# Optimization experiments

Measured on AMD Instinct MI355X. Metric: run time of the kernel, lower is better.

Reference implementation:

```python
import jax, jax.numpy as jnp
import numpy as np

NH = 16
NKV = 4
ROPE_BASE = 10000.0
ROPE_TSL = 1024
EPS = 1.1920928955078125e-07  # torch fp32 finfo eps (F.rms_norm default)


def _rms_norm(t):
    return t * jax.lax.rsqrt(jnp.mean(t * t, axis=-1, keepdims=True) + EPS)


def _rope_tables(T, hd):
    # Rotary with rd = hd (rope_dims=0 -> full-head rope). NTK rescale if T > tsl.
    rd = hd
    if T > ROPE_TSL:
        base = ROPE_BASE * (T / ROPE_TSL) ** (rd / (rd - 2))
    else:
        base = ROPE_BASE
    inv_freq = 1.0 / base ** (np.arange(0, rd, 2, dtype=np.float32) / rd)
    t = np.arange(T, dtype=np.float32)
    fr = np.outer(t, inv_freq)  # [T, hd//2]
    return jnp.asarray(np.cos(fr)), jnp.asarray(np.sin(fr))


def _apply_rope(x, cos, sin):
    # x: [B,T,H,D]; cos/sin: [T, D//2] broadcast over batch & heads
    h = x.shape[-1] // 2
    x1, x2 = x[..., :h], x[..., h:]
    c = cos[None, :, None, :]
    s = sin[None, :, None, :]
    return jnp.concatenate((x1 * c + x2 * s, -x1 * s + x2 * c), axis=-1)


def setup_inputs() -> dict:
    key = jax.random.key(0)
    k1, k2, k3, k4, k5 = jax.random.split(key, 5)
    B, T, dim = 2, 2048, 2048
    hd = dim // NH
    kd = NKV * hd
    std = 0.02
    return {
        "x": jax.random.normal(k1, (B, T, dim), dtype=jnp.float32),
        "Wq": jax.random.normal(k2, (dim, dim), dtype=jnp.float32) * std,
        "Wk": jax.random.normal(k3, (kd, dim), dtype=jnp.float32) * std,
        "Wv": jax.random.normal(k4, (kd, dim), dtype=jnp.float32) * std,
        "Wp": jax.random.normal(k5, (dim, dim), dtype=jnp.float32) * std,
        "q_gain": jnp.full((NH,), 1.5, dtype=jnp.float32),
    }


def reference(x, Wq, Wk, Wv, Wp, q_gain):
    B, T, d = x.shape
    hd = d // NH
    g = NH // NKV
    q = (x @ Wq.T).reshape(B, T, NH, hd)
    k = (x @ Wk.T).reshape(B, T, NKV, hd)
    v = (x @ Wv.T).reshape(B, T, NKV, hd)
    q = _rms_norm(q)
    k = _rms_norm(k)
    cos, sin = _rope_tables(T, hd)
    q = _apply_rope(q, cos, sin)
    k = _apply_rope(k, cos, sin)
    q = q * q_gain[None, None, :, None]
    # GQA causal SDPA: group queries per kv head
    qg = q.reshape(B, T, NKV, g, hd)
    scores = jnp.einsum("btkgd,bskd->bkgts", qg, k) / jnp.sqrt(jnp.asarray(hd, x.dtype))
    causal = jnp.tril(jnp.ones((T, T), dtype=bool))
    scores = jnp.where(causal[None, None, None, :, :], scores, jnp.asarray(-jnp.inf, scores.dtype))
    attn = jax.nn.softmax(scores, axis=-1)
    y = jnp.einsum("bkgts,bskd->btkgd", attn, v).reshape(B, T, d)
    return y @ Wp.T
```

## Files before the change

kernel.cpp:

```cpp
#include <hip/hip_runtime.h>
#include <math.h>

#define NH 16
#define NKV 4
#define HD 128
#define DIM 2048
#define GQ 4
#define EPS 1.1920928955078125e-07f

typedef unsigned short u16;
using bf16x8 = __attribute__((ext_vector_type(8))) short;
using f16x4  = __attribute__((ext_vector_type(4))) _Float16;
using f32x4  = __attribute__((ext_vector_type(4))) float;

__device__ inline float fast_exp2(float x) { return __builtin_amdgcn_exp2f(x); }

__device__ inline short f2bf(float f) {
    unsigned u = __builtin_bit_cast(unsigned, f);
    return (short)((u + 0x7FFFu + ((u >> 16) & 1u)) >> 16);
}
__device__ inline u16 f2h(float f) {
    _Float16 h = (_Float16)f;
    return __builtin_bit_cast(u16, h);
}

#define ASYNC_LOAD16(g, l)                                                        \
    __builtin_amdgcn_global_load_lds(                                             \
        (const __attribute__((address_space(1))) unsigned*)(g),                   \
        (__attribute__((address_space(3))) unsigned*)(l), 16, 0, 0)

#define SCHED_FENCE() __builtin_amdgcn_sched_barrier(0)
#define WAIT_LGKM0()  asm volatile("s_waitcnt lgkmcnt(0)" ::: "memory")
#define WAIT_VM(N)    asm volatile("s_waitcnt vmcnt(" #N ")" ::: "memory")

__global__ __launch_bounds__(256) void cvt_fused(
    const float* __restrict__ x,  const float* __restrict__ wq,
    const float* __restrict__ wk, const float* __restrict__ wv,
    const float* __restrict__ wp,
    u16* __restrict__ x16, u16* __restrict__ wqkv, u16* __restrict__ wp16,
    float* __restrict__ ct, float* __restrict__ st, float l2b64,
    int nx4, int total, int nblk_cvt) {
    if ((int)blockIdx.x >= nblk_cvt) {
        const int idx = (blockIdx.x - nblk_cvt) * 256 + threadIdx.x;
        const int t = idx >> 6;
        const int j = idx & 63;
        const float inv_freq = fast_exp2(-(float)j * l2b64);
        const float fr = (float)t * inv_freq;
        ct[idx] = cosf(fr);
        st[idx] = sinf(fr);
        return;
    }
    int i = blockIdx.x * 256 + threadIdx.x;
    if (i >= total) return;
    const int nw4 = DIM * DIM / 4;
    const int nk4 = (NKV * HD) * DIM / 4;
    const float4* s4;
    ushort4* d4;
    if (i < nx4) {
        s4 = (const float4*)x + i; d4 = (ushort4*)x16 + i;
    } else {
        int j = i - nx4;
        if (j < nw4) {
            s4 = (const float4*)wq + j; d4 = (ushort4*)wqkv + j;
        } else {
            j -= nw4;
            if (j < nk4) {
                s4 = (const float4*)wk + j;
                d4 = (ushort4*)wqkv + (size_t)2048 * DIM / 4 + j;
            } else {
                j -= nk4;
                if (j < nk4) {
                    s4 = (const float4*)wv + j;
                    d4 = (ushort4*)wqkv + (size_t)2560 * DIM / 4 + j;
                } else {
                    j -= nk4;
                    s4 = (const float4*)wp + j; d4 = (ushort4*)wp16 + j;
                }
            }
        }
    }
    float4 f = *s4;
    ushort4 o;
    o.x = (u16)f2bf(f.x); o.y = (u16)f2bf(f.y);
    o.z = (u16)f2bf(f.z); o.w = (u16)f2bf(f.w);
    *d4 = o;
}

#define BN 256
#define BKT 64
#define NKT (DIM / BKT)

template <int EPI, int MT>
__global__ __launch_bounds__(512, 2) void gemm256(
    const u16* __restrict__ A, const u16* __restrict__ W,
    float* __restrict__ C, int N,
    u16* __restrict__ q16, u16* __restrict__ k16,
    u16* __restrict__ vt16,
    const float* __restrict__ ctab, const float* __restrict__ stab,
    const float* __restrict__ q_gain, int T) {
    __shared__ u16 As[2][MT * 64 * BKT];
    __shared__ u16 Bs[2][BN * BKT];

    const int tid  = threadIdx.x;
    const int wid  = tid >> 6;
    const int lane = tid & 63;
    const int l16  = lane & 15;
    const int quad = lane >> 4;
    const int wm   = wid >> 1;
    const int wn   = wid & 1;
    const int m0   = blockIdx.x * (MT * 64);
    const int n0   = blockIdx.y * BN;
    const int K    = DIM;

    const int srow = lane >> 3;
    const int scol = ((lane & 7) ^ srow) * 8;
    const u16* pa = A + (size_t)(m0 + srow) * K + scol;
    const u16* pw = W + (size_t)(n0 + srow) * K + scol;

    const int ca0 = ((quad)     ^ (l16 & 7)) * 8;
    const int ca1 = ((4 + quad) ^ (l16 & 7)) * 8;

    f32x4 acc[MT][8];
#pragma unroll
    for (int i = 0; i < MT; i++)
#pragma unroll
        for (int j = 0; j < 8; j++) acc[i][j] = (f32x4){0.f, 0.f, 0.f, 0.f};

#pragma unroll
    for (int r = 0; r < MT; r++)
        ASYNC_LOAD16(pa + (size_t)(r * 64 + wid * 8) * K, &As[0][(r * 64 + wid * 8) * BKT]);
    ASYNC_LOAD16(pw + (size_t)(0 * 64 + wid * 8) * K, &Bs[0][(0 * 64 + wid * 8) * BKT]);
    ASYNC_LOAD16(pw + (size_t)(2 * 64 + wid * 8) * K, &Bs[0][(2 * 64 + wid * 8) * BKT]);
    ASYNC_LOAD16(pw + (size_t)(1 * 64 + wid * 8) * K, &Bs[0][(1 * 64 + wid * 8) * BKT]);
    ASYNC_LOAD16(pw + (size_t)(3 * 64 + wid * 8) * K, &Bs[0][(3 * 64 + wid * 8) * BKT]);
    WAIT_VM(2);
    SCHED_FENCE();
    __builtin_amdgcn_s_barrier();
    SCHED_FENCE();

#pragma unroll 1
    for (int kt = 0; kt < NKT; kt++) {
        const int cur = kt & 1;
        const u16* Ac = &As[cur][0];
        const u16* Bc = &Bs[cur][0];
        u16* An = &As[cur ^ 1][0];
        u16* Bn = &Bs[cur ^ 1][0];
        const size_t ko = (size_t)((kt + 1) & (NKT - 1)) * BKT;

        bf16x8 a0[MT], a1[MT];

        {
            bf16x8 bf[4];
#pragma unroll
            for (int mt = 0; mt < MT; mt++)
                a0[mt] = *(const bf16x8*)&Ac[(wm * (MT * 16) + mt * 16 + l16) * BKT + ca0];
#pragma unroll
            for (int nt = 0; nt < 4; nt++)
                bf[nt] = *(const bf16x8*)&Bc[(wn * 128 + nt * 16 + l16) * BKT + ca0];
#pragma unroll
            for (int r = 0; r < MT; r++)
                ASYNC_LOAD16(pa + (size_t)(r * 64 + wid * 8) * K + ko,
                             &An[(r * 64 + wid * 8) * BKT]);
            SCHED_FENCE();
            __builtin_amdgcn_s_barrier();
            WAIT_LGKM0();
            SCHED_FENCE();
            __builtin_amdgcn_s_setprio(1);
#pragma unroll
            for (int mt = 0; mt < MT; mt++)
#pragma unroll
                for (int nt = 0; nt < 4; nt++)
                    acc[mt][nt] = __builtin_amdgcn_mfma_f32_16x16x32_bf16(
                        a0[mt], bf[nt], acc[mt][nt], 0, 0, 0);
            __builtin_amdgcn_s_setprio(0);
        }

        {
            bf16x8 bf[4];
#pragma unroll
            for (int mt = 0; mt < MT; mt++)
                a1[mt] = *(const bf16x8*)&Ac[(wm * (MT * 16) + mt * 16 + l16) * BKT + ca1];
#pragma unroll
            for (int nt = 0; nt < 4; nt++)
                bf[nt] = *(const bf16x8*)&Bc[(wn * 128 + nt * 16 + l16) * BKT + ca1];
            ASYNC_LOAD16(pw + (size_t)(0 * 64 + wid * 8) * K + ko,
                         &Bn[(0 * 64 + wid * 8) * BKT]);
            ASYNC_LOAD16(pw + (size_t)(2 * 64 + wid * 8) * K + ko,
                         &Bn[(2 * 64 + wid * 8) * BKT]);
            SCHED_FENCE();
            __builtin_amdgcn_s_barrier();
            WAIT_LGKM0();
            SCHED_FENCE();
            __builtin_amdgcn_s_setprio(1);
#pragma unroll
            for (int mt = 0; mt < MT; mt++)
#pragma unroll
                for (int nt = 0; nt < 4; nt++)
                    acc[mt][nt] = __builtin_amdgcn_mfma_f32_16x16x32_bf16(
                        a1[mt], bf[nt], acc[mt][nt], 0, 0, 0);
            __builtin_amdgcn_s_setprio(0);
            if constexpr (MT == 4) { WAIT_VM(6); } else { WAIT_VM(4); }
            SCHED_FENCE();
            __builtin_amdgcn_s_barrier();
            SCHED_FENCE();
        }

        {
            bf16x8 bf[4];
#pragma unroll
            for (int nt = 0; nt < 4; nt++)
                bf[nt] = *(const bf16x8*)&Bc[(wn * 128 + (nt + 4) * 16 + l16) * BKT + ca0];
            ASYNC_LOAD16(pw + (size_t)(1 * 64 + wid * 8) * K + ko,
                         &Bn[(1 * 64 + wid * 8) * BKT]);
            ASYNC_LOAD16(pw + (size_t)(3 * 64 + wid * 8) * K + ko,
                         &Bn[(3 * 64 + wid * 8) * BKT]);
            SCHED_FENCE();
            __builtin_amdgcn_s_barrier();
            WAIT_LGKM0();
            SCHED_FENCE();
            __builtin_amdgcn_s_setprio(1);
#pragma unroll
            for (int mt = 0; mt < MT; mt++)
#pragma unroll
                for (int nt = 0; nt < 4; nt++)
                    acc[mt][nt + 4] = __builtin_amdgcn_mfma_f32_16x16x32_bf16(
                        a0[mt], bf[nt], acc[mt][nt + 4], 0, 0, 0);
            __builtin_amdgcn_s_setprio(0);
        }

        {
            bf16x8 bf[4];
#pragma unroll
            for (int nt = 0; nt < 4; nt++)
                bf[nt] = *(const bf16x8*)&Bc[(wn * 128 + (nt + 4) * 16 + l16) * BKT + ca1];
            SCHED_FENCE();
            __builtin_amdgcn_s_barrier();
            WAIT_LGKM0();
            SCHED_FENCE();
            __builtin_amdgcn_s_setprio(1);
#pragma unroll
            for (int mt = 0; mt < MT; mt++)
#pragma unroll
                for (int nt = 0; nt < 4; nt++)
                    acc[mt][nt + 4] = __builtin_amdgcn_mfma_f32_16x16x32_bf16(
                        a1[mt], bf[nt], acc[mt][nt + 4], 0, 0, 0);
            __builtin_amdgcn_s_setprio(0);
            WAIT_VM(2);
            SCHED_FENCE();
            __builtin_amdgcn_s_barrier();
            SCHED_FENCE();
        }
    }
    WAIT_VM(0);

    if constexpr (EPI == 0) {
#pragma unroll
        for (int mt = 0; mt < MT; mt++)
#pragma unroll
            for (int nt = 0; nt < 8; nt++)
#pragma unroll
                for (int r = 0; r < 4; r++)
                    C[(size_t)(m0 + wm * (MT * 16) + mt * 16 + quad * 4 + r) * N +
                      n0 + wn * 128 + nt * 16 + l16] = acc[mt][nt][r];
    } else {
        const int nb = n0 + wn * 128;
        if (nb < 2560) {
            const bool isQ = (nb < 2048);
            const float gval =
                isQ ? (q_gain[nb >> 7] * 0.08838834764831843f * 1.4426950408889634f)
                    : 1.0f;
#pragma unroll
            for (int mt = 0; mt < MT; mt++) {
#pragma unroll
                for (int r = 0; r < 4; r++) {
                    float s = 0.f;
#pragma unroll
                    for (int nt = 0; nt < 8; nt++) {
                        float a = acc[mt][nt][r];
                        s = fmaf(a, a, s);
                    }
                    s += __shfl_xor(s, 1);
                    s += __shfl_xor(s, 2);
                    s += __shfl_xor(s, 4);
                    s += __shfl_xor(s, 8);
                    const float scale = rsqrtf(s * (1.0f / HD) + EPS) * gval;
                    const int m = m0 + wm * (MT * 16) + mt * 16 + quad * 4 + r;
                    const int t = m & (T - 1);
                    const float* ct = ctab + t * 64;
                    const float* st = stab + t * 64;
                    u16* dst = isQ ? (q16 + (size_t)m * 2048 + nb)
                                   : (k16 + (size_t)m * 512 + (nb - 2048));
#pragma unroll
                    for (int nt = 0; nt < 4; nt++) {
                        const int j = nt * 16 + l16;
                        const float c = ct[j], sn = st[j];
                        const float x1 = acc[mt][nt][r] * scale;
                        const float x2 = acc[mt][nt + 4][r] * scale;
                        dst[j]      = (u16)f2bf(x1 * c + x2 * sn);
                        dst[j + 64] = (u16)f2bf(x2 * c - x1 * sn);
                    }
                }
            }
        } else {
#pragma unroll
            for (int mt = 0; mt < MT; mt++) {
                const int mb = m0 + wm * (MT * 16) + mt * 16 + quad * 4;
                const int b = mb >> 11;
                const int t0 = mb & (T - 1);
#pragma unroll
                for (int nt = 0; nt < 8; nt++) {
                    const int dcol = nb - 2560 + nt * 16 + l16;
                    const int kvh = dcol >> 7;
                    const int d = dcol & (HD - 1);
                    ushort4 o;
                    o.x = f2h(acc[mt][nt][0]);
                    o.y = f2h(acc[mt][nt][1]);
                    o.z = f2h(acc[mt][nt][2]);
                    o.w = f2h(acc[mt][nt][3]);
                    *(ushort4*)(vt16 + ((size_t)((b * NKV + kvh) * HD + d)) * T + t0) = o;
                }
            }
        }
    }
}

#define QT 128
#define SK 64

__global__ __launch_bounds__(512) void flash5(const u16* __restrict__ q16,
                                              const u16* __restrict__ k16,
                                              const u16* __restrict__ vt16,
                                              u16* __restrict__ y16, int T) {
    __shared__ u16 Ks[2][SK * 128];
    __shared__ u16 Vt[2][HD * 64];

    const int tid = threadIdx.x;
    const int wave = tid >> 6;
    const int lane = tid & 63;
    const int l16 = lane & 15;
    const int quad = lane >> 4;

    const int bid = blockIdx.x;
    const int bh = bid & 31;
    const int qi = bid >> 5;
    const int nqt = T / QT;
    const int qt = (qi < (nqt >> 1)) ? qi : (nqt - 1 - (qi - (nqt >> 1)));
    const int h = bh & 15;
    const int b = bh >> 4;
    const int kv = h / GQ;

    const u16* kg = k16 + ((size_t)b * T * NKV + kv) * HD;
    const u16* vg = vt16 + (size_t)(b * NKV + kv) * HD * T;

    const int krow_in_seg = lane >> 4;
    const int kclog_base = lane & 15;
    const int vrow_in_seg = lane >> 3;
    const int vclog = (lane & 7) ^ (lane >> 3);

    const int q0 = qt * QT;
    const int qglob = q0 + wave * 16 + l16;
    const int nts = q0 / SK + 2;

    bf16x8 qf[4];
    {
        const u16* qp = q16 + ((size_t)(b * T + qglob) * NH + h) * HD;
#pragma unroll
        for (int kc = 0; kc < 4; kc++)
            qf[kc] = *(const bf16x8*)(qp + kc * 32 + quad * 8);
    }

    f32x4 of[8];
#pragma unroll
    for (int i = 0; i < 8; i++) of[i] = (f32x4){0.f, 0.f, 0.f, 0.f};
    float m_i = -1e30f, l_i = 0.0f;

#pragma unroll
    for (int j = 0; j < 2; j++) {
        const int seg = wave * 2 + j;
        const int r = seg * 4 + krow_in_seg;
        const int clog = kclog_base ^ (r & 15);
        ASYNC_LOAD16(kg + (size_t)r * (NKV * HD) + clog * 8, &Ks[0][seg * 512]);
        const int d = seg * 8 + vrow_in_seg;
        ASYNC_LOAD16(vg + (size_t)d * T + vclog * 8, &Vt[0][seg * 512]);
    }

    for (int it = 0; it < nts; it++) {
        const int cur = it & 1;
        __syncthreads();

        if (it + 1 < nts) {
            const int s1 = (it + 1) * SK;
#pragma unroll
            for (int j = 0; j < 2; j++) {
                const int seg = wave * 2 + j;
                const int r = seg * 4 + krow_in_seg;
                const int clog = kclog_base ^ (r & 15);
                ASYNC_LOAD16(kg + (size_t)(s1 + r) * (NKV * HD) + clog * 8,
                             &Ks[cur ^ 1][seg * 512]);
                const int d = seg * 8 + vrow_in_seg;
                ASYNC_LOAD16(vg + (size_t)d * T + s1 + vclog * 8,
                             &Vt[cur ^ 1][seg * 512]);
            }
        }

        if (it == nts - 1 && wave < 4) continue;

        f32x4 sf[4];
#pragma unroll
        for (int st = 0; st < 4; st++) sf[st] = (f32x4){0.f, 0.f, 0.f, 0.f};
#pragma unroll
        for (int kc = 0; kc < 4; kc++)
#pragma unroll
            for (int st = 0; st < 4; st++) {
                const int row = st * 16 + l16;
                bf16x8 kf = *(const bf16x8*)
                    &Ks[cur][row * 128 + (((kc * 4 + quad) ^ l16) * 8)];
                sf[st] = __builtin_amdgcn_mfma_f32_16x16x32_bf16(kf, qf[kc], sf[st], 0, 0, 0);
            }

        if (it >= nts - 2) {
            const int s0 = it * SK;
#pragma unroll
            for (int st = 0; st < 4; st++)
#pragma unroll
                for (int r = 0; r < 4; r++)
                    if (s0 + st * 16 + quad * 4 + r > qglob) sf[st][r] = -1e30f;
        }

        float tm = -1e30f;
#pragma unroll
        for (int st = 0; st < 4; st++)
#pragma unroll
            for (int r = 0; r < 4; r++) tm = fmaxf(tm, sf[st][r]);
        tm = fmaxf(tm, __shfl_xor(tm, 16));
        tm = fmaxf(tm, __shfl_xor(tm, 32));

        if (__ballot(tm > m_i + 8.0f)) {
            const float mnew = fmaxf(m_i, tm);
            const float alpha = fast_exp2(m_i - mnew);
            m_i = mnew;
            l_i *= alpha;
#pragma unroll
            for (int dt = 0; dt < 8; dt++)
#pragma unroll
                for (int r = 0; r < 4; r++) of[dt][r] *= alpha;
        }

        f16x4 pf[4];
        float ls = 0.0f;
#pragma unroll
        for (int st = 0; st < 4; st++)
#pragma unroll
            for (int r = 0; r < 4; r++) {
                float e = fast_exp2(sf[st][r] - m_i);
                ls += e;
                pf[st][r] = (_Float16)e;
            }
        ls += __shfl_xor(ls, 16);
        ls += __shfl_xor(ls, 32);
        l_i += ls;

#pragma unroll
        for (int st = 0; st < 4; st++) {
            const int clog = st * 2 + (quad >> 1);
#pragma unroll
            for (int dt = 0; dt < 8; dt++) {
                const int d = dt * 16 + l16;
                const int phys = clog ^ (l16 & 7);
                f16x4 va = *(const f16x4*)
                    &Vt[cur][d * 64 + phys * 8 + (quad & 1) * 4];
                of[dt] = __builtin_amdgcn_mfma_f32_16x16x16f16(va, pf[st], of[dt], 0, 0, 0);
            }
        }
    }

    const float inv = 1.0f / l_i;
    u16* yp = y16 + ((size_t)(b * T + qglob) * NH + h) * HD + quad * 4;
#pragma unroll
    for (int dt = 0; dt < 8; dt++) {
        ushort4 o;
        o.x = (u16)f2bf(of[dt][0] * inv);
        o.y = (u16)f2bf(of[dt][1] * inv);
        o.z = (u16)f2bf(of[dt][2] * inv);
        o.w = (u16)f2bf(of[dt][3] * inv);
        *(ushort4*)(yp + dt * 16) = o;
    }
}

extern "C" void kernel_launch(void* const* d_in, const int* in_sizes, int n_in,
                              void* d_out, int out_size, void* d_ws, size_t ws_size,
                              hipStream_t stream) {
    const float* x      = (const float*)d_in[0];
    const float* Wq     = (const float*)d_in[1];
    const float* Wk     = (const float*)d_in[2];
    const float* Wv     = (const float*)d_in[3];
    const float* Wp     = (const float*)d_in[4];
    const float* q_gain = (const float*)d_in[5];
    float* out = (float*)d_out;

    const int B = 2;
    const int BT = in_sizes[0] / DIM;
    const int T = BT / B;
    const int KD = NKV * HD;

    u16* x16   = (u16*)d_ws;
    u16* wqkv  = x16 + (size_t)BT * DIM;
    u16* wp16  = wqkv + (size_t)3072 * DIM;
    u16* q16   = wp16 + (size_t)DIM * DIM;
    u16* k16   = q16 + (size_t)BT * DIM;
    u16* vt16  = k16 + (size_t)BT * KD;
    float* ctab = (float*)(vt16 + (size_t)BT * KD);
    float* stab = ctab + (size_t)T * 64;
    u16* y16   = x16;

    double base = 10000.0;
    if (T > 1024) base = 10000.0 * pow((double)T / 1024.0, 128.0 / 126.0);
    const float l2b64 = (float)(log2(base) / 64.0);

    const int nx4  = BT * DIM / 4;
    const int total4 = nx4 + 2 * (DIM * DIM / 4) + 2 * (KD * DIM / 4);
    const int nblk_cvt = (total4 + 255) / 256;
    const int nblk_rope = (T * 64 + 255) / 256;

    cvt_fused<<<nblk_cvt + nblk_rope, 256, 0, stream>>>(
        x, Wq, Wk, Wv, Wp, x16, wqkv, wp16, ctab, stab, l2b64, nx4, total4, nblk_cvt);

    gemm256<1, 4><<<dim3(BT / 256, 3072 / BN), 512, 0, stream>>>(
        x16, wqkv, nullptr, 0, q16, k16, vt16, ctab, stab, q_gain, T);

    flash5<<<32 * (T / QT), 512, 0, stream>>>(q16, k16, vt16, y16, T);

    gemm256<0, 2><<<dim3(BT / 128, DIM / BN), 512, 0, stream>>>(
        y16, wp16, out, DIM, nullptr, nullptr, nullptr, nullptr, nullptr, nullptr, T);
}
```

Before: 303.1 us.

## Prefetch next GEMM fragment from LDS during current MFMA phase

Restructures the GEMM main loop into a register-level software pipeline. Each phase now issues the LDS reads for the next phase's A/B fragments before running its MFMAs, and the first fragments of the next K-tile are loaded at the end of the current tile. This is meant to hide LDS read latency behind matrix-core work. In exchange it uses more live registers, and it reorders the vmcnt waits and barriers, which risks a race on the double-buffered LDS or extra barrier overhead.

```diff
diff --git a/kernel.cpp b/kernel.cpp
--- a/kernel.cpp
+++ b/kernel.cpp
@@ -126,6 +126,8 @@
 #pragma unroll
         for (int j = 0; j < 8; j++) acc[i][j] = (f32x4){0.f, 0.f, 0.f, 0.f};
 
+    bf16x8 a0[MT], a1[MT], bA[4], bB[4], bC[4], bD[4];
+
 #pragma unroll
     for (int r = 0; r < MT; r++)
         ASYNC_LOAD16(pa + (size_t)(r * 64 + wid * 8) * K, &As[0][(r * 64 + wid * 8) * BKT]);
@@ -137,26 +139,25 @@
     SCHED_FENCE();
     __builtin_amdgcn_s_barrier();
     SCHED_FENCE();
+#pragma unroll
+    for (int mt = 0; mt < MT; mt++)
+        a0[mt] = *(const bf16x8*)&As[0][(wm * (MT * 16) + mt * 16 + l16) * BKT + ca0];
+#pragma unroll
+    for (int nt = 0; nt < 4; nt++)
+        bA[nt] = *(const bf16x8*)&Bs[0][(wn * 128 + nt * 16 + l16) * BKT + ca0];
 
 #pragma unroll 1
     for (int kt = 0; kt < NKT; kt++) {
         const int cur = kt & 1;
         const u16* Ac = &As[cur][0];
         const u16* Bc = &Bs[cur][0];
+        const u16* Anr = &As[cur ^ 1][0];
+        const u16* Bnr = &Bs[cur ^ 1][0];
         u16* An = &As[cur ^ 1][0];
         u16* Bn = &Bs[cur ^ 1][0];
         const size_t ko = (size_t)((kt + 1) & (NKT - 1)) * BKT;
 
-        bf16x8 a0[MT], a1[MT];
-
         {
-            bf16x8 bf[4];
-#pragma unroll
-            for (int mt = 0; mt < MT; mt++)
-                a0[mt] = *(const bf16x8*)&Ac[(wm * (MT * 16) + mt * 16 + l16) * BKT + ca0];
-#pragma unroll
-            for (int nt = 0; nt < 4; nt++)
-                bf[nt] = *(const bf16x8*)&Bc[(wn * 128 + nt * 16 + l16) * BKT + ca0];
 #pragma unroll
             for (int r = 0; r < MT; r++)
                 ASYNC_LOAD16(pa + (size_t)(r * 64 + wid * 8) * K + ko,
@@ -165,24 +166,27 @@
             __builtin_amdgcn_s_barrier();
             WAIT_LGKM0();
             SCHED_FENCE();
+#pragma unroll
+            for (int mt = 0; mt < MT; mt++)
+                a1[mt] = *(const bf16x8*)&Ac[(wm * (MT * 16) + mt * 16 + l16) * BKT + ca1];
+#pragma unroll
+            for (int nt = 0; nt < 4; nt++)
+                bB[nt] = *(const bf16x8*)&Bc[(wn * 128 + nt * 16 + l16) * BKT + ca1];
+            SCHED_FENCE();
             __builtin_amdgcn_s_setprio(1);
 #pragma unroll
             for (int mt = 0; mt < MT; mt++)
 #pragma unroll
                 for (int nt = 0; nt < 4; nt++)
                     acc[mt][nt] = __builtin_amdgcn_mfma_f32_16x16x32_bf16(
-                        a0[mt], bf[nt], acc[mt][nt], 0, 0, 0);
+                        a0[mt], bA[nt], acc[mt][nt], 0, 0, 0);
             __builtin_amdgcn_s_setprio(0);
+            if constexpr (MT == 4) { WAIT_VM(4); } else { WAIT_VM(2); }
+            SCHED_FENCE();
+            __builtin_amdgcn_s_barrier();
         }
 
         {
-            bf16x8 bf[4];
-#pragma unroll
-            for (int mt = 0; mt < MT; mt++)
-                a1[mt] = *(const bf16x8*)&Ac[(wm * (MT * 16) + mt * 16 + l16) * BKT + ca1];
-#pragma unroll
-            for (int nt = 0; nt < 4; nt++)
-                bf[nt] = *(const bf16x8*)&Bc[(wn * 128 + nt * 16 + l16) * BKT + ca1];
             ASYNC_LOAD16(pw + (size_t)(0 * 64 + wid * 8) * K + ko,
                          &Bn[(0 * 64 + wid * 8) * BKT]);
             ASYNC_LOAD16(pw + (size_t)(2 * 64 + wid * 8) * K + ko,
@@ -191,25 +195,23 @@
             __builtin_amdgcn_s_barrier();
             WAIT_LGKM0();
             SCHED_FENCE();
+#pragma unroll
+            for (int nt = 0; nt < 4; nt++)
+                bC[nt] = *(const bf16x8*)&Bc[(wn * 128 + (nt + 4) * 16 + l16) * BKT + ca0];
+            SCHED_FENCE();
             __builtin_amdgcn_s_setprio(1);
 #pragma unroll
             for (int mt = 0; mt < MT; mt++)
 #pragma unroll
                 for (int nt = 0; nt < 4; nt++)
                     acc[mt][nt] = __builtin_amdgcn_mfma_f32_16x16x32_bf16(
-                        a1[mt], bf[nt], acc[mt][nt], 0, 0, 0);
+                        a1[mt], bB[nt], acc[mt][nt], 0, 0, 0);
             __builtin_amdgcn_s_setprio(0);
-            if constexpr (MT == 4) { WAIT_VM(6); } else { WAIT_VM(4); }
-            SCHED_FENCE();
-            __builtin_amdgcn_s_barrier();
-            SCHED_FENCE();
+            SCHED_FENCE();
+            __builtin_amdgcn_s_barrier();
         }
 
         {
-            bf16x8 bf[4];
-#pragma unroll
-            for (int nt = 0; nt < 4; nt++)
-                bf[nt] = *(const bf16x8*)&Bc[(wn * 128 + (nt + 4) * 16 + l16) * BKT + ca0];
             ASYNC_LOAD16(pw + (size_t)(1 * 64 + wid * 8) * K + ko,
                          &Bn[(1 * 64 + wid * 8) * BKT]);
             ASYNC_LOAD16(pw + (size_t)(3 * 64 + wid * 8) * K + ko,
@@ -218,24 +220,34 @@
             __builtin_amdgcn_s_barrier();
             WAIT_LGKM0();
             SCHED_FENCE();
+#pragma unroll
+            for (int nt = 0; nt < 4; nt++)
+                bD[nt] = *(const bf16x8*)&Bc[(wn * 128 + (nt + 4) * 16 + l16) * BKT + ca1];
+            SCHED_FENCE();
             __builtin_amdgcn_s_setprio(1);
 #pragma unroll
             for (int mt = 0; mt < MT; mt++)
 #pragma unroll
                 for (int nt = 0; nt < 4; nt++)
                     acc[mt][nt + 4] = __builtin_amdgcn_mfma_f32_16x16x32_bf16(
-                        a0[mt], bf[nt], acc[mt][nt + 4], 0, 0, 0);
+                        a0[mt], bC[nt], acc[mt][nt + 4], 0, 0, 0);
             __builtin_amdgcn_s_setprio(0);
+            WAIT_VM(2);
+            SCHED_FENCE();
+            __builtin_amdgcn_s_barrier();
         }
 
         {
-            bf16x8 bf[4];
+            SCHED_FENCE();
+            __builtin_amdgcn_s_barrier();
+            WAIT_LGKM0();
+            SCHED_FENCE();
+#pragma unroll
+            for (int mt = 0; mt < MT; mt++)
+                a0[mt] = *(const bf16x8*)&Anr[(wm * (MT * 16) + mt * 16 + l16) * BKT + ca0];
 #pragma unroll
             for (int nt = 0; nt < 4; nt++)
-                bf[nt] = *(const bf16x8*)&Bc[(wn * 128 + (nt + 4) * 16 + l16) * BKT + ca1];
-            SCHED_FENCE();
-            __builtin_amdgcn_s_barrier();
-            WAIT_LGKM0();
+                bA[nt] = *(const bf16x8*)&Bnr[(wn * 128 + nt * 16 + l16) * BKT + ca0];
             SCHED_FENCE();
             __builtin_amdgcn_s_setprio(1);
 #pragma unroll
@@ -243,12 +255,10 @@
 #pragma unroll
                 for (int nt = 0; nt < 4; nt++)
                     acc[mt][nt + 4] = __builtin_amdgcn_mfma_f32_16x16x32_bf16(
-                        a1[mt], bf[nt], acc[mt][nt + 4], 0, 0, 0);
+                        a1[mt], bD[nt], acc[mt][nt + 4], 0, 0, 0);
             __builtin_amdgcn_s_setprio(0);
-            WAIT_VM(2);
-            SCHED_FENCE();
-            __builtin_amdgcn_s_barrier();
-            SCHED_FENCE();
+            SCHED_FENCE();
+            __builtin_amdgcn_s_barrier();
         }
     }
     WAIT_VM(0);
```

Measured after the change: 341.6 us. 12.7% more time.

## Restructure GEMM mainloop into 4-stage BK=32 async pipeline with one barrier per step

Applied to the files above, without the earlier changes.

Replaces the double-buffered BK=64 GEMM mainloop, which had four sub-phases and several barriers per tile, with a 4-deep ring of BK=32 LDS buffers. Loads are prefetched three tiles ahead, and each iteration uses a single barrier and vmcnt wait. The LDS swizzle and load mapping are redone for the 32-wide tiles. The aim is to hide global-load latency better and cut barrier and sync overhead. The trade-off is half as much MFMA work per barrier, and each LDS fragment is used for fewer MFMAs.

```diff
diff --git a/kernel.cpp b/kernel.cpp
--- a/kernel.cpp
+++ b/kernel.cpp
@@ -30,7 +30,6 @@
         (__attribute__((address_space(3))) unsigned*)(l), 16, 0, 0)
 
 #define SCHED_FENCE() __builtin_amdgcn_sched_barrier(0)
-#define WAIT_LGKM0()  asm volatile("s_waitcnt lgkmcnt(0)" ::: "memory")
 #define WAIT_VM(N)    asm volatile("s_waitcnt vmcnt(" #N ")" ::: "memory")
 
 __global__ __launch_bounds__(256) void cvt_fused(
@@ -87,19 +86,19 @@
 }
 
 #define BN 256
-#define BKT 64
-#define NKT (DIM / BKT)
+#define BKT2 32
+#define NT2 (DIM / BKT2)
 
 template <int EPI, int MT>
-__global__ __launch_bounds__(512, 2) void gemm256(
+__global__ __launch_bounds__(512, 2) void gemm32(
     const u16* __restrict__ A, const u16* __restrict__ W,
     float* __restrict__ C, int N,
     u16* __restrict__ q16, u16* __restrict__ k16,
     u16* __restrict__ vt16,
     const float* __restrict__ ctab, const float* __restrict__ stab,
     const float* __restrict__ q_gain, int T) {
-    __shared__ u16 As[2][MT * 64 * BKT];
-    __shared__ u16 Bs[2][BN * BKT];
+    __shared__ u16 As[4][MT * 64 * BKT2];
+    __shared__ u16 Bs[4][BN * BKT2];
 
     const int tid  = threadIdx.x;
     const int wid  = tid >> 6;
@@ -112,13 +111,12 @@
     const int n0   = blockIdx.y * BN;
     const int K    = DIM;
 
-    const int srow = lane >> 3;
-    const int scol = ((lane & 7) ^ srow) * 8;
-    const u16* pa = A + (size_t)(m0 + srow) * K + scol;
-    const u16* pw = W + (size_t)(n0 + srow) * K + scol;
-
-    const int ca0 = ((quad)     ^ (l16 & 7)) * 8;
-    const int ca1 = ((4 + quad) ^ (l16 & 7)) * 8;
+    const int srow = tid >> 2;
+    const int sc   = (((tid & 3) ^ (srow & 3)) * 8);
+    const u16* pa = A + (size_t)(m0 + srow) * K + sc;
+    const u16* pw = W + (size_t)(n0 + srow) * K + sc;
+
+    const int ca = (quad ^ (l16 & 3)) * 8;
 
     f32x4 acc[MT][8];
 #pragma unroll
@@ -127,129 +125,60 @@
         for (int j = 0; j < 8; j++) acc[i][j] = (f32x4){0.f, 0.f, 0.f, 0.f};
 
 #pragma unroll
-    for (int r = 0; r < MT; r++)
-        ASYNC_LOAD16(pa + (size_t)(r * 64 + wid * 8) * K, &As[0][(r * 64 + wid * 8) * BKT]);
-    ASYNC_LOAD16(pw + (size_t)(0 * 64 + wid * 8) * K, &Bs[0][(0 * 64 + wid * 8) * BKT]);
-    ASYNC_LOAD16(pw + (size_t)(2 * 64 + wid * 8) * K, &Bs[0][(2 * 64 + wid * 8) * BKT]);
-    ASYNC_LOAD16(pw + (size_t)(1 * 64 + wid * 8) * K, &Bs[0][(1 * 64 + wid * 8) * BKT]);
-    ASYNC_LOAD16(pw + (size_t)(3 * 64 + wid * 8) * K, &Bs[0][(3 * 64 + wid * 8) * BKT]);
-    WAIT_VM(2);
+    for (int p = 0; p < 3; p++) {
+        const size_t ko = (size_t)p * BKT2;
+        u16* Ab = &As[p][0];
+        u16* Bb = &Bs[p][0];
+        ASYNC_LOAD16(pa + ko, Ab + tid * 8);
+        if constexpr (MT == 4) {
+            ASYNC_LOAD16(pa + (size_t)128 * K + ko, Ab + tid * 8 + 4096);
+        }
+        ASYNC_LOAD16(pw + ko, Bb + tid * 8);
+        ASYNC_LOAD16(pw + (size_t)128 * K + ko, Bb + tid * 8 + 4096);
+    }
+    if constexpr (MT == 4) { WAIT_VM(8); } else { WAIT_VM(6); }
     SCHED_FENCE();
     __builtin_amdgcn_s_barrier();
     SCHED_FENCE();
 
 #pragma unroll 1
-    for (int kt = 0; kt < NKT; kt++) {
-        const int cur = kt & 1;
-        const u16* Ac = &As[cur][0];
-        const u16* Bc = &Bs[cur][0];
-        u16* An = &As[cur ^ 1][0];
-        u16* Bn = &Bs[cur ^ 1][0];
-        const size_t ko = (size_t)((kt + 1) & (NKT - 1)) * BKT;
-
-        bf16x8 a0[MT], a1[MT];
+    for (int kt = 0; kt < NT2; kt++) {
+        const u16* Ab = &As[kt & 3][0];
+        const u16* Bb = &Bs[kt & 3][0];
 
         {
-            bf16x8 bf[4];
-#pragma unroll
-            for (int mt = 0; mt < MT; mt++)
-                a0[mt] = *(const bf16x8*)&Ac[(wm * (MT * 16) + mt * 16 + l16) * BKT + ca0];
-#pragma unroll
-            for (int nt = 0; nt < 4; nt++)
-                bf[nt] = *(const bf16x8*)&Bc[(wn * 128 + nt * 16 + l16) * BKT + ca0];
-#pragma unroll
-            for (int r = 0; r < MT; r++)
-                ASYNC_LOAD16(pa + (size_t)(r * 64 + wid * 8) * K + ko,
-                             &An[(r * 64 + wid * 8) * BKT]);
-            SCHED_FENCE();
-            __builtin_amdgcn_s_barrier();
-            WAIT_LGKM0();
-            SCHED_FENCE();
-            __builtin_amdgcn_s_setprio(1);
-#pragma unroll
-            for (int mt = 0; mt < MT; mt++)
-#pragma unroll
-                for (int nt = 0; nt < 4; nt++)
-                    acc[mt][nt] = __builtin_amdgcn_mfma_f32_16x16x32_bf16(
-                        a0[mt], bf[nt], acc[mt][nt], 0, 0, 0);
-            __builtin_amdgcn_s_setprio(0);
-        }
-
-        {
-            bf16x8 bf[4];
-#pragma unroll
-            for (int mt = 0; mt < MT; mt++)
-                a1[mt] = *(const bf16x8*)&Ac[(wm * (MT * 16) + mt * 16 + l16) * BKT + ca1];
-#pragma unroll
-            for (int nt = 0; nt < 4; nt++)
-                bf[nt] = *(const bf16x8*)&Bc[(wn * 128 + nt * 16 + l16) * BKT + ca1];
-            ASYNC_LOAD16(pw + (size_t)(0 * 64 + wid * 8) * K + ko,
-                         &Bn[(0 * 64 + wid * 8) * BKT]);
-            ASYNC_LOAD16(pw + (size_t)(2 * 64 + wid * 8) * K + ko,
-                         &Bn[(2 * 64 + wid * 8) * BKT]);
-            SCHED_FENCE();
-            __builtin_amdgcn_s_barrier();
-            WAIT_LGKM0();
-            SCHED_FENCE();
-            __builtin_amdgcn_s_setprio(1);
-#pragma unroll
-            for (int mt = 0; mt < MT; mt++)
-#pragma unroll
-                for (int nt = 0; nt < 4; nt++)
-                    acc[mt][nt] = __builtin_amdgcn_mfma_f32_16x16x32_bf16(
-                        a1[mt], bf[nt], acc[mt][nt], 0, 0, 0);
-            __builtin_amdgcn_s_setprio(0);
-            if constexpr (MT == 4) { WAIT_VM(6); } else { WAIT_VM(4); }
-            SCHED_FENCE();
-            __builtin_amdgcn_s_barrier();
-            SCHED_FENCE();
-        }
-
-        {
-            bf16x8 bf[4];
-#pragma unroll
-            for (int nt = 0; nt < 4; nt++)
-                bf[nt] = *(const bf16x8*)&Bc[(wn * 128 + (nt + 4) * 16 + l16) * BKT + ca0];
-            ASYNC_LOAD16(pw + (size_t)(1 * 64 + wid * 8) * K + ko,
-                         &Bn[(1 * 64 + wid * 8) * BKT]);
-            ASYNC_LOAD16(pw + (size_t)(3 * 64 + wid * 8) * K + ko,
-                         &Bn[(3 * 64 + wid * 8) * BKT]);
-            SCHED_FENCE();
-            __builtin_amdgcn_s_barrier();
-            WAIT_LGKM0();
-            SCHED_FENCE();
-            __builtin_amdgcn_s_setprio(1);
-#pragma unroll
-            for (int mt = 0; mt < MT; mt++)
-#pragma unroll
-                for (int nt = 0; nt < 4; nt++)
-                    acc[mt][nt + 4] = __builtin_amdgcn_mfma_f32_16x16x32_bf16(
-                        a0[mt], bf[nt], acc[mt][nt + 4], 0, 0, 0);
-            __builtin_amdgcn_s_setprio(0);
-        }
-
-        {
-            bf16x8 bf[4];
-#pragma unroll
-            for (int nt = 0; nt < 4; nt++)
-                bf[nt] = *(const bf16x8*)&Bc[(wn * 128 + (nt + 4) * 16 + l16) * BKT + ca1];
-            SCHED_FENCE();
-            __builtin_amdgcn_s_barrier();
-            WAIT_LGKM0();
-            SCHED_FENCE();
-            __builtin_amdgcn_s_setprio(1);
-#pragma unroll
-            for (int mt = 0; mt < MT; mt++)
-#pragma unroll
-                for (int nt = 0; nt < 4; nt++)
-                    acc[mt][nt + 4] = __builtin_amdgcn_mfma_f32_16x16x32_bf16(
-                        a1[mt], bf[nt], acc[mt][nt + 4], 0, 0, 0);
-            __builtin_amdgcn_s_setprio(0);
-            WAIT_VM(2);
-            SCHED_FENCE();
-            __builtin_amdgcn_s_barrier();
-            SCHED_FENCE();
-        }
+            const size_t ko = (size_t)((kt + 3) & (NT2 - 1)) * BKT2;
+            u16* An = &As[(kt + 3) & 3][0];
+            u16* Bn = &Bs[(kt + 3) & 3][0];
+            ASYNC_LOAD16(pa + ko, An + tid * 8);
+            if constexpr (MT == 4) {
+                ASYNC_LOAD16(pa + (size_t)128 * K + ko, An + tid * 8 + 4096);
+            }
+            ASYNC_LOAD16(pw + ko, Bn + tid * 8);
+            ASYNC_LOAD16(pw + (size_t)128 * K + ko, Bn + tid * 8 + 4096);
+        }
+
+        bf16x8 af[MT], bf[8];
+#pragma unroll
+        for (int mt = 0; mt < MT; mt++)
+            af[mt] = *(const bf16x8*)&Ab[(wm * (MT * 16) + mt * 16 + l16) * BKT2 + ca];
+#pragma unroll
+        for (int nt = 0; nt < 8; nt++)
+            bf[nt] = *(const bf16x8*)&Bb[(wn * 128 + nt * 16 + l16) * BKT2 + ca];
+
+        __builtin_amdgcn_s_setprio(1);
+#pragma unroll
+        for (int mt = 0; mt < MT; mt++)
+#pragma unroll
+            for (int nt = 0; nt < 8; nt++)
+                acc[mt][nt] = __builtin_amdgcn_mfma_f32_16x16x32_bf16(
+                    af[mt], bf[nt], acc[mt][nt], 0, 0, 0);
+        __builtin_amdgcn_s_setprio(0);
+
+        if constexpr (MT == 4) { WAIT_VM(8); } else { WAIT_VM(6); }
+        SCHED_FENCE();
+        __builtin_amdgcn_s_barrier();
+        SCHED_FENCE();
     }
     WAIT_VM(0);
 
@@ -525,11 +454,11 @@
     cvt_fused<<<nblk_cvt + nblk_rope, 256, 0, stream>>>(
         x, Wq, Wk, Wv, Wp, x16, wqkv, wp16, ctab, stab, l2b64, nx4, total4, nblk_cvt);
 
-    gemm256<1, 4><<<dim3(BT / 256, 3072 / BN), 512, 0, stream>>>(
+    gemm32<1, 4><<<dim3(BT / 256, 3072 / BN), 512, 0, stream>>>(
         x16, wqkv, nullptr, 0, q16, k16, vt16, ctab, stab, q_gain, T);
 
     flash5<<<32 * (T / QT), 512, 0, stream>>>(q16, k16, vt16, y16, T);
 
-    gemm256<0, 2><<<dim3(BT / 128, DIM / BN), 512, 0, stream>>>(
+    gemm32<0, 2><<<dim3(BT / 128, DIM / BN), 512, 0, stream>>>(
         y16, wp16, out, DIM, nullptr, nullptr, nullptr, nullptr, nullptr, nullptr, T);
 }
```

Result: slower. 331.3 us (+9.3%).
